# Performance work log

Measured on AMD Instinct MI355X. Metric: run time of the kernel, lower is better.

The kernel has to match this reference:

```python
import jax, jax.numpy as jnp
import numpy as np

N, E = 20000, 320000
C, IN_NF, HID_NF, OUT_NF, CH_NF, RAD_NF = 14, 128, 128, 128, 16, 128
CONSTANT = 1.0
LN_EPS = 1e-5
SCALE = 0.02


def _pool_matrix(c, dtype):
    # RollerPooling buffer: pool_matrix[i] averages a sliding window of size c-i
    ones = np.ones((c, c), dtype=np.float32)
    mats = [(np.triu(ones) - np.triu(ones, k=c - i)) / float(c - i) for i in range(c)]
    return jnp.asarray(np.stack(mats), dtype=dtype)


def setup_inputs() -> dict:
    key = jax.random.key(0)
    ks = jax.random.split(key, 32)
    h = jax.random.normal(ks[0], (N, IN_NF), jnp.float32)
    x = jax.random.normal(ks[1], (N, C, 3), jnp.float32)
    row = jax.random.randint(ks[2], (E,), 0, N)
    off = jax.random.randint(ks[3], (E,), 1, N)
    col = (row + off) % N  # guarantees row != col (avoids zero-distance edges)
    channel_attr = jax.random.normal(ks[4], (N, C, CH_NF), jnp.float32)
    w = jax.random.uniform(ks[5], (N, C), jnp.float32, 0.1, 1.0)
    keep = jax.random.uniform(ks[6], (N, C)) > 0.3
    keep = keep.at[:, 0].set(True)  # every node has >=1 active channel
    channel_weights = w * keep.astype(jnp.float32)

    def lin(k, o, i):
        k1, k2 = jax.random.split(k)
        return (jax.random.normal(k1, (o, i), jnp.float32) * SCALE,
                jax.random.normal(k2, (o,), jnp.float32) * SCALE)

    radial_W, radial_b = lin(ks[7], RAD_NF, CH_NF * CH_NF)
    e1_W, e1_b = lin(ks[8], HID_NF, 2 * IN_NF + RAD_NF)
    e2_W, e2_b = lin(ks[9], HID_NF, HID_NF)
    att_W, att_b = lin(ks[10], 1, HID_NF)
    c1_W, c1_b = lin(ks[11], HID_NF, HID_NF)
    c2_W, c2_b = lin(ks[12], C, HID_NF)
    n1_W, n1_b = lin(ks[13], HID_NF, IN_NF + HID_NF)
    n2_W, n2_b = lin(ks[14], OUT_NF, HID_NF)
    ln_g = jnp.ones((OUT_NF,), jnp.float32)
    ln_b = jnp.zeros((OUT_NF,), jnp.float32)
    return dict(h=h, x=x, row=row, col=col, channel_attr=channel_attr,
                channel_weights=channel_weights,
                radial_W=radial_W, radial_b=radial_b,
                e1_W=e1_W, e1_b=e1_b, e2_W=e2_W, e2_b=e2_b,
                att_W=att_W, att_b=att_b,
                c1_W=c1_W, c1_b=c1_b, c2_W=c2_W, c2_b=c2_b,
                n1_W=n1_W, n1_b=n1_b, n2_W=n2_W, n2_b=n2_b,
                ln_g=ln_g, ln_b=ln_b)


def _scatter_mean(v, idx, n):
    s = jnp.zeros((n,) + v.shape[1:], v.dtype).at[idx].add(v)
    cnt = jnp.zeros((n,), v.dtype).at[idx].add(1.0)
    cnt = jnp.maximum(cnt, 1.0)
    return s / cnt.reshape((n,) + (1,) * (v.ndim - 1))


def _forward(h, x, row, col, channel_attr, channel_weights,
             radial_W, radial_b, e1_W, e1_b, e2_W, e2_b, att_W, att_b,
             c1_W, c1_b, c2_W, c2_b, n1_W, n1_b, n2_W, n2_b, ln_g, ln_b):
    n, c, d = x.shape
    silu = jax.nn.silu
    coord_r = x[row]           # [E, C, 3]
    coord_c = x[col]
    # pairwise channel distances [E, C, C]
    dist = jnp.linalg.norm(coord_r[:, :, None, :] - coord_c[:, None, :, :], axis=-1)
    cw_r = channel_weights[row]
    cw_c = channel_weights[col]
    coord_msg = dist * (cw_r[:, :, None] * cw_c[:, None, :])
    # attr_r^T @ coord_msg @ attr_c -> [E, CH_NF, CH_NF]
    radial = jnp.einsum('eca,ecd,edb->eab', channel_attr[row], coord_msg, channel_attr[col])
    radial = radial.reshape(radial.shape[0], -1)
    rnorm = jnp.linalg.norm(radial, axis=-1, keepdims=True) + CONSTANT
    radial = (radial @ radial_W.T + radial_b) / rnorm  # [E, RAD_NF]
    # pooled column coord over active channels
    mask = (channel_weights != 0).astype(x.dtype)      # [N, C]
    csum = mask.sum(-1)                                # [N]
    pooled_col = (coord_c * mask[col][:, :, None]).sum(1) / csum[col][:, None]  # [E, 3]
    coord_diff = coord_r - pooled_col[:, None, :]      # [E, C, 3]
    # edge MLP (dropout = identity in eval)
    ef = jnp.concatenate([h[row], h[col], radial], axis=-1)
    ef = silu(ef @ e1_W.T + e1_b)
    ef = silu(ef @ e2_W.T + e2_b)
    ef = ef * jax.nn.sigmoid(ef @ att_W.T + att_b)     # att_mlp (hidden_nf == input_nf)
    # coord MLP + roller pooling
    ch = silu(ef @ c1_W.T + c1_b) @ c2_W.T + c2_b      # [E, C]
    tsize = csum[row].astype(jnp.int32) - 1            # [E] in [0, C-1]
    pool_mat = _pool_matrix(c, x.dtype)                # [C, C, C]
    pooled = jnp.einsum('eij,ej->ei', pool_mat[tsize], ch)  # [E, C]
    trans = coord_diff * pooled[:, :, None]            # [E, C, 3]
    x_out = x + _scatter_mean(trans, row, n)
    agg = _scatter_mean(ef, col, n)
    nh = jnp.concatenate([h, agg], axis=-1)
    nh = silu(nh @ n1_W.T + n1_b) @ n2_W.T + n2_b
    y = h + nh
    mu = y.mean(-1, keepdims=True)
    var = ((y - mu) ** 2).mean(-1, keepdims=True)
    h_out = (y - mu) / jnp.sqrt(var + LN_EPS) * ln_g + ln_b
    return h_out, x_out


def reference(h, x, row, col, channel_attr, channel_weights,
              radial_W, radial_b, e1_W, e1_b, e2_W, e2_b, att_W, att_b,
              c1_W, c1_b, c2_W, c2_b, n1_W, n1_b, n2_W, n2_b, ln_g, ln_b):
    return _forward(h, x, row, col, channel_attr, channel_weights,
                    radial_W, radial_b, e1_W, e1_b, e2_W, e2_b, att_W, att_b,
                    c1_W, c1_b, c2_W, c2_b, n1_W, n1_b, n2_W, n2_b, ln_g, ln_b)
```

## Files before the change

### kernel.cpp

```cpp
#include <hip/hip_runtime.h>
#include <math.h>

#define NN 20000
#define NE 320000

typedef const float* fp;
typedef short short8 __attribute__((ext_vector_type(8)));
typedef short short4v __attribute__((ext_vector_type(4)));
typedef float f32x4 __attribute__((ext_vector_type(4)));

__device__ __forceinline__ short F2B(float f) {
    unsigned u = __float_as_uint(f);
    return (short)((u + 0x7fffu + ((u >> 16) & 1u)) >> 16);
}
__device__ __forceinline__ short F2Bf(float f) {
    return (short)((__float_as_uint(f) + 0x8000u) >> 16);
}
__device__ __forceinline__ float B2F(short s) {
    return __uint_as_float(((unsigned)(unsigned short)s) << 16);
}
__device__ __forceinline__ float siluf(float v) { return v / (1.f + __expf(-v)); }
__device__ __forceinline__ f32x4 ld4(const float* p) {
    f32x4 v;
    __builtin_memcpy(&v, p, 16);
// ... 117 lines not shown
        wb[i] = F2B(v);
        return;
    }
    b -= 584;
    if (b < 128) {
        int o = b, k = tid;
        float acc = 0.f;
        for (int m = 0; m < 128; m++) acc += e1W[o * 384 + 256 + m] * rW[m * 256 + k];
        wb[32768 + o * 256 + k] = F2B(acc);
        if (k == 0) {
            float bsum = 0.f;
            for (int m = 0; m < 128; m++) bsum += e1W[o * 384 + 256 + m] * rB[m];
            bc[o] = bsum;
        }
        return;
    }
    b -= 128;
    if (b < 10000) {
        int i = b * 256 + tid;
        hb[i] = F2B(h[i]);
        return;
    }
    b -= 10000;
    if (b < 79) {
        int n = b * 256 + tid;
        if (n >= NN) return;
        float cnt = 0.f, px = 0.f, py = 0.f, pz = 0.f;
#pragma unroll
        for (int c = 0; c < 14; c++) {
            float w = cw[n * 14 + c];
            if (w != 0.f) {
                cnt += 1.f;
                px += x[(n * 14 + c) * 3 + 0];
                py += x[(n * 14 + c) * 3 + 1];
                pz += x[(n * 14 + c) * 3 + 2];
            }
        }
        if (cnt < 1.f) cnt = 1.f;
        csum[n] = cnt;
        pool[n * 3 + 0] = px / cnt;
        pool[n * 3 + 1] = py / cnt;
        pool[n * 3 + 2] = pz / cnt;
        return;
    }
    b -= 79;
    {
        int i = b * 256 + tid;
        int n = i >> 8, rem = i & 255, c = rem >> 4, a = rem & 15;
        float v = (c < 14) ? attr[(size_t)n * 224 + c * 16 + a] * cw[n * 14 + c] : 0.f;
        aT[(size_t)n * 256 + a * 16 + c] = F2B(v);
    }
}

__global__ void k_scan(int* __restrict__ cnt0, int* __restrict__ cnt1,
                       int* __restrict__ off0, int* __restrict__ off1) {
    __shared__ int part[256];
    const int tid = threadIdx.x;
    for (int a = 0; a < 2; a++) {
        int* cnt = a ? cnt1 : cnt0;
        int* off = a ? off1 : off0;
        int c0 = tid * 79, c1 = c0 + 79;
        if (c1 > 20000) c1 = 20000;
        int s = 0;
        for (int i = c0; i < c1; i++) s += cnt[i];
        part[tid] = s;
        __syncthreads();
        if (tid == 0) {
            int r = 0;
            for (int i = 0; i < 256; i++) { int t = part[i]; part[i] = r; r += t; }
        }
        __syncthreads();
        int run = part[tid];
        for (int i = c0; i < c1; i++) {
            int cv = cnt[i];
            off[i] = run;
            cnt[i] = run;
            run += cv;
        }
        if (tid == 255) off[20000] = run;
        __syncthreads();
    }
}

__global__ void k_fill(const int* __restrict__ row, const int* __restrict__ col,
                       int* __restrict__ head_r, int* __restrict__ head_c,
                       int* __restrict__ rpos,
                       int* __restrict__ row_s, int* __restrict__ col_s) {
    int e = blockIdx.x * 256 + threadIdx.x;
    if (e >= NE) return;
    int r = row[e], c = col[e];
    int pc = atomicAdd(&head_c[c], 1);
    row_s[pc] = r;
    col_s[pc] = c;
    int pr = atomicAdd(&head_r[r], 1);
    rpos[pc] = pr;
}

__device__ __forceinline__ void gemm_lds(const short* __restrict__ A, int sA,
                                         const short* __restrict__ W, int Ws, int K,
                                         int mt, int nt0, int nts, f32x4* acc) {
    const int lane = threadIdx.x & 63;
    const short* ap = A + (mt * 16 + (lane & 15)) * sA + ((lane >> 4) * 8);
    for (int k0 = 0; k0 < K; k0 += 32) {
        short8 a = *(const short8*)(ap + k0);
#pragma unroll
        for (int t = 0; t < nts; t++) {
            short8 b = *(const short8*)(W + ((nt0 + t) * 16 + (lane & 15)) * Ws + k0 + ((lane >> 4) * 8));
            acc[t] = __builtin_amdgcn_mfma_f32_16x16x32_bf16(a, b, acc[t], 0, 0, 0);
        }
    }
}
__device__ __forceinline__ void gemm_grow(const short* __restrict__ arow,
                                          const short* __restrict__ W, int Ws, int K,
                                          int nt0, int nts, f32x4* acc) {
    const int lane = threadIdx.x & 63;
    for (int k0 = 0; k0 < K; k0 += 32) {
        short8 a = *(const short8*)(arow + k0);
#pragma unroll
        for (int t = 0; t < nts; t++) {
            short8 b = *(const short8*)(W + ((nt0 + t) * 16 + (lane & 15)) * Ws + k0 + ((lane >> 4) * 8));
            acc[t] = __builtin_amdgcn_mfma_f32_16x16x32_bf16(a, b, acc[t], 0, 0, 0);
        }
    }
}

__global__ __launch_bounds__(256, 4) void k_hw(const short* __restrict__ hb,
                                               const short* __restrict__ wb,
                                               short* __restrict__ H12) {
    __shared__ __attribute__((aligned(16))) short A[32 * 136];
    const int tid = threadIdx.x, lane = tid & 63, w = tid >> 6;
    const int bb = lane & 15, quad = lane >> 4;
    const int mt = w & 1, nh = w >> 1, nb0 = blockIdx.x * 32;
    for (int p = tid; p < 512; p += 256) {
        int i = p >> 4, v = p & 15;
        *(short8*)(A + i * 136 + v * 8) = *(const short8*)(hb + (size_t)(nb0 + i) * 128 + v * 8);
    }
    __syncthreads();
    f32x4 acc[4];
#pragma unroll
    for (int t = 0; t < 4; t++) acc[t] = (f32x4){0.f, 0.f, 0.f, 0.f};
    gemm_lds(A, 136, wb, 256, 128, mt, nh * 4, 4, acc);
#pragma unroll
    for (int t = 0; t < 4; t++)
#pragma unroll
        for (int i = 0; i < 4; i++) {
            int m = mt * 16 + quad * 4 + i, n = (nh * 4 + t) * 16 + bb;
            H12[(size_t)(nb0 + m) * 256 + n] = F2Bf(acc[t][i]);
        }
#pragma unroll
    for (int t = 0; t < 4; t++) acc[t] = (f32x4){0.f, 0.f, 0.f, 0.f};
    gemm_lds(A, 136, wb + 128, 256, 128, mt, nh * 4, 4, acc);
#pragma unroll
    for (int t = 0; t < 4; t++)
#pragma unroll
        for (int i = 0; i < 4; i++) {
            int m = mt * 16 + quad * 4 + i, n = (nh * 4 + t) * 16 + bb;
            H12[(size_t)(nb0 + m) * 256 + 128 + n] = F2Bf(acc[t][i]);
        }
}

__global__ __launch_bounds__(256, 7) void k_edge(
    fp x, const int* __restrict__ row_s, const int* __restrict__ col_s,
    const int* __restrict__ rpos,
    const short* __restrict__ attrT, const short* __restrict__ H12,
    const short* __restrict__ wb, const float* __restrict__ bc,
    fp e1B, fp e2B, fp aW, fp aB, fp c1B, fp c2B,
    const float* __restrict__ csum, const float* __restrict__ poolc,
    short* __restrict__ e1p, short* __restrict__ pooledb,
    float* __restrict__ pcrec) {
    __shared__ __attribute__((aligned(16))) short U[8704];
    __shared__ float s_inv[32];
    __shared__ int s_r[32], s_c[32];
    __shared__ float s_ch[32][14];
    __shared__ float s_ps[32][15];
    __shared__ float s_red8[32][8], s_gate[32];

    const int tid = threadIdx.x, lane = tid & 63, w = tid >> 6;
    const int bb = lane & 15, quad = lane >> 4;
    const int mt = w & 1, nh = w >> 1;
    const int e0 = blockIdx.x * 32;
    const short* Wc = wb + 32768;
    short* Ar = U;
    short* V1 = U;
    short* V2 = U + 4352;

    if (tid < 32) { s_r[tid] = row_s[e0 + tid]; s_c[tid] = col_s[e0 + tid]; }
    __syncthreads();

    const int iic = bb < 14 ? bb : 13;
    const bool q3 = (quad == 3);
    const int cb = q3 ? 30 : quad * 12;
#pragma unroll 2
    for (int m = 0; m < 8; m++) {
        const int ei = w * 8 + m;
        const int r = s_r[ei], c = s_c[ei];
        short4v arv = *(const short4v*)(attrT + (size_t)r * 256 + bb * 16 + quad * 4);
        short4v acv = *(const short4v*)(attrT + (size_t)c * 256 + bb * 16 + quad * 4);
        const float* xrp = x + (size_t)r * 42 + iic * 3;
        float xr0 = xrp[0], xr1 = xrp[1], xr2 = xrp[2];
        const float* xcp = x + (size_t)c * 42 + cb;
        f32x4 L0 = ld4(xcp), L1 = ld4(xcp + 4), L2 = ld4(xcp + 8);
        float cxv[4], cyv[4], czv[4];
        cxv[0] = q3 ? L1[2] : L0[0]; cyv[0] = q3 ? L1[3] : L0[1]; czv[0] = q3 ? L2[0] : L0[2];
        cxv[1] = q3 ? L2[1] : L0[3]; cyv[1] = q3 ? L2[2] : L1[0]; czv[1] = q3 ? L2[3] : L1[1];
        cxv[2] = q3 ? L2[1] : L1[2]; cyv[2] = q3 ? L2[2] : L1[3]; czv[2] = q3 ? L2[3] : L2[0];
        cxv[3] = L2[1];              cyv[3] = L2[2];              czv[3] = L2[3];
        short4v msgv;
#pragma unroll
        for (int t = 0; t < 4; t++) {
            float dx = xr0 - cxv[t], dy = xr1 - cyv[t], dz = xr2 - czv[t];
            msgv[t] = F2Bf(sqrtf(dx * dx + dy * dy + dz * dz));
        }
        f32x4 t2 = mfma16(msgv, acv, (f32x4){0.f, 0.f, 0.f, 0.f});
        short4v t2v;
#pragma unroll
        for (int g = 0; g < 4; g++) t2v[g] = F2Bf(t2[g]);
        f32x4 rad = mfma16(arv, t2v, (f32x4){0.f, 0.f, 0.f, 0.f});
        float ss = rad[0] * rad[0] + rad[1] * rad[1] + rad[2] * rad[2] + rad[3] * rad[3];
#pragma unroll
        for (int off = 32; off > 0; off >>= 1) ss += __shfl_xor(ss, off, 64);
        float inv = 1.f / (sqrtf(ss) + 1.f);
        if (lane == 0) s_inv[ei] = inv;
#pragma unroll
        for (int g = 0; g < 4; g++)
            Ar[ei * 264 + (quad * 4 + g) * 16 + bb] = F2Bf(rad[g] * inv);
    }
    __syncthreads();

    f32x4 racc[2][2];
#pragma unroll
    for (int a = 0; a < 2; a++)
#pragma unroll
        for (int b = 0; b < 2; b++) racc[a][b] = (f32x4){0.f, 0.f, 0.f, 0.f};
    for (int k0 = 0; k0 < 256; k0 += 32) {
        short8 a0 = *(const short8*)(Ar + bb * 264 + k0 + quad * 8);
        short8 a1 = *(const short8*)(Ar + (16 + bb) * 264 + k0 + quad * 8);
        short8 b0 = *(const short8*)(Wc + (size_t)(w * 32 + bb) * 256 + k0 + quad * 8);
        short8 b1 = *(const short8*)(Wc + (size_t)(w * 32 + 16 + bb) * 256 + k0 + quad * 8);
        racc[0][0] = __builtin_amdgcn_mfma_f32_16x16x32_bf16(a0, b0, racc[0][0], 0, 0, 0);
        racc[0][1] = __builtin_amdgcn_mfma_f32_16x16x32_bf16(a0, b1, racc[0][1], 0, 0, 0);
        racc[1][0] = __builtin_amdgcn_mfma_f32_16x16x32_bf16(a1, b0, racc[1][0], 0, 0, 0);
        racc[1][1] = __builtin_amdgcn_mfma_f32_16x16x32_bf16(a1, b1, racc[1][1], 0, 0, 0);
    }
    __syncthreads();

#pragma unroll
    for (int a = 0; a < 2; a++)
#pragma unroll
        for (int b = 0; b < 2; b++)
#pragma unroll
            for (int i = 0; i < 4; i++) {
                int m = a * 16 + quad * 4 + i, n = w * 32 + b * 16 + bb;
                V1[m * 136 + n] = F2Bf(racc[a][b][i] + s_inv[m] * bc[n]);
            }
    __syncthreads();

    for (int p = tid; p < 512; p += 256) {
        int e = p >> 4, v = p & 15;
        short8 hr = *(const short8*)(H12 + (size_t)s_r[e] * 256 + v * 8);
        short8 hc = *(const short8*)(H12 + (size_t)s_c[e] * 256 + 128 + v * 8);
        short8 pp = *(const short8*)(V1 + e * 136 + v * 8);
        short8 o;
#pragma unroll
        for (int j = 0; j < 8; j++)
            o[j] = F2Bf(siluf(B2F(hr[j]) + B2F(hc[j]) + B2F(pp[j]) + e1B[v * 8 + j]));
        *(short8*)(V1 + e * 136 + v * 8) = o;
    }
    __syncthreads();

    f32x4 acc[4];
#pragma unroll
    for (int t = 0; t < 4; t++) acc[t] = (f32x4){0.f, 0.f, 0.f, 0.f};
    gemm_lds(V1, 136, wb + 65536, 128, 128, mt, nh * 4, 4, acc);
#pragma unroll
    for (int t = 0; t < 4; t++)
#pragma unroll
        for (int i = 0; i < 4; i++) {
            int m = mt * 16 + quad * 4 + i, n = (nh * 4 + t) * 16 + bb;
            V2[m * 136 + n] = F2Bf(siluf(acc[t][i] + e2B[n]));
        }
    __syncthreads();

    {
        int e = tid >> 3, j = tid & 7;
        float s = 0.f;
        for (int f = j * 16; f < j * 16 + 16; f++) s += B2F(V2[e * 136 + f]) * aW[f];
        s_red8[e][j] = s;
    }
    __syncthreads();
    if (tid < 32) {
        float s = 0.f;
#pragma unroll
        for (int j = 0; j < 8; j++) s += s_red8[tid][j];
        s_gate[tid] = 1.f / (1.f + __expf(-(s + aB[0])));
    }
#pragma unroll
    for (int t = 0; t < 4; t++) acc[t] = (f32x4){0.f, 0.f, 0.f, 0.f};
    gemm_lds(V2, 136, wb + 81920, 128, 128, mt, nh * 4, 4, acc);
    __syncthreads();

#pragma unroll
    for (int t = 0; t < 4; t++)
#pragma unroll
        for (int i = 0; i < 4; i++) {
            int m = mt * 16 + quad * 4 + i, n = (nh * 4 + t) * 16 + bb;
            V1[m * 136 + n] = F2Bf(siluf(s_gate[m] * acc[t][i] + c1B[n]));
        }
    for (int p = tid; p < 512; p += 256) {
        int e = p >> 4, v = p & 15;
        short8 a = *(const short8*)(V2 + e * 136 + v * 8);
        short8 o;
#pragma unroll
        for (int j = 0; j < 8; j++) o[j] = F2Bf(B2F(a[j]) * s_gate[e]);
        *(short8*)(e1p + (size_t)(e0 + e) * 128 + v * 8) = o;
    }
    __syncthreads();

    if (nh == 0) {
        f32x4 a4 = (f32x4){0.f, 0.f, 0.f, 0.f};
        gemm_lds(V1, 136, wb + 98304, 128, 128, mt, 0, 1, &a4);
#pragma unroll
        for (int i = 0; i < 4; i++) {
            int m = mt * 16 + quad * 4 + i;
            if (bb < 14) s_ch[m][bb] = a4[i] + c2B[bb];
        }
    }
    __syncthreads();

    if (tid < 32) {
        int t = (int)(csum[s_r[tid]] + 0.5f) - 1;
        if (t < 0) t = 0; if (t > 13) t = 13;
        int Wd = 14 - t;
        float run = 0.f;
        s_ps[tid][0] = 0.f;
        for (int j = 0; j < 14; j++) { run += s_ch[tid][j]; s_ps[tid][j + 1] = run; }
        float invW = 1.f / (float)Wd;
        int rp = rpos[e0 + tid];
        for (int i = 0; i < 14; i++) {
            int jend = i + Wd; if (jend > 14) jend = 14;
            pooledb[(size_t)rp * 14 + i] = F2Bf((s_ps[tid][jend] - s_ps[tid][i]) * invW);
        }
        int c = s_c[tid];
        float4 pc = make_float4(poolc[c * 3 + 0], poolc[c * 3 + 1], poolc[c * 3 + 2], 0.f);
        *(float4*)(pcrec + (size_t)rp * 4) = pc;
    }
}

__global__ __launch_bounds__(256, 3) void k_edge_fused(
    fp x, const int* __restrict__ row, const int* __restrict__ col,
    fp attr, fp cw, const short* __restrict__ hb, const short* __restrict__ wb,
    fp e1B, fp e2B, fp aW, fp aB, fp c1B, fp c2B,
    const float* __restrict__ bc, const float* __restrict__ csum,
    const float* __restrict__ poolc,
    float* __restrict__ xacc, float* __restrict__ agg,
    float* __restrict__ cntr, float* __restrict__ cntc) {
    __shared__ __attribute__((aligned(16))) short R1[13056];
    __shared__ float s_xr2[32 * 42];
    __shared__ float T[4][352];
    __shared__ int   s_r[32], s_c[32];
    __shared__ float s_inv[32];
    __shared__ float s_ch[32][14], s_pool[32][14];
    __shared__ float s_red8[32][8];
    __shared__ float s_gate[32];

    const int tid = threadIdx.x, lane = tid & 63, w = tid >> 6;
    const int bb = lane & 15, quad = lane >> 4;

    if (tid < 32) { s_r[tid] = row[blockIdx.x * 32 + tid]; s_c[tid] = col[blockIdx.x * 32 + tid]; }
    __syncthreads();

    float* slot = T[w];
    float* t2w = slot + 72;
    for (int i8 = 0; i8 < 8; i8++) {
        const int e = w * 8 + i8;
        const int r = s_r[e], cl = s_c[e];
        if (lane < 42) {
            s_xr2[e * 42 + lane] = x[(size_t)r * 42 + lane];
            slot[lane] = x[(size_t)cl * 42 + lane];
        }
        if (lane < 14)      slot[42 + lane] = cw[r * 14 + lane];
        else if (lane < 28) slot[56 + (lane - 14)] = cw[cl * 14 + (lane - 14)];
        __builtin_amdgcn_wave_barrier();

        const int iic = bb < 14 ? bb : 13;
        float xr0 = s_xr2[e * 42 + iic * 3], xr1 = s_xr2[e * 42 + iic * 3 + 1],
              xr2v = s_xr2[e * 42 + iic * 3 + 2];
        float cwri = slot[42 + iic];
        short8 msgv, acv;
#pragma unroll
        for (int t = 0; t < 8; t++) {
            int jj = quad * 8 + t, jc = jj < 14 ? jj : 13;
            float dx = xr0 - slot[jc * 3], dy = xr1 - slot[jc * 3 + 1], dz = xr2v - slot[jc * 3 + 2];
            float m = sqrtf(dx * dx + dy * dy + dz * dz) * cwri * slot[56 + jc];
            msgv[t] = (bb < 14 && jj < 14) ? F2B(m) : (short)0;
            acv[t] = F2B(attr[(size_t)cl * 224 + jc * 16 + bb]);
        }
        f32x4 t2 = (f32x4){0.f, 0.f, 0.f, 0.f};
        t2 = __builtin_amdgcn_mfma_f32_16x16x32_bf16(msgv, acv, t2, 0, 0, 0);
#pragma unroll
        for (int g = 0; g < 4; g++) t2w[(quad * 4 + g) * 17 + bb] = t2[g];
        __builtin_amdgcn_wave_barrier();

        short8 arv, t2v;
#pragma unroll
        for (int t = 0; t < 8; t++) {
            int kk = quad * 8 + t, kc = kk < 16 ? kk : 15;
            t2v[t] = F2B(t2w[kc * 17 + bb]);
            arv[t] = (kk < 14) ? F2B(attr[(size_t)r * 224 + kk * 16 + bb]) : (short)0;
        }
        f32x4 rad = (f32x4){0.f, 0.f, 0.f, 0.f};
        rad = __builtin_amdgcn_mfma_f32_16x16x32_bf16(arv, t2v, rad, 0, 0, 0);

// ... 39 lines not shown
    gemm_lds(V1, 136, wb + 65536, 128, 128, mt, nh * 4, 4, acc);
    __syncthreads();
#pragma unroll
    for (int t = 0; t < 4; t++)
#pragma unroll
        for (int i = 0; i < 4; i++) {
            int m = mt * 16 + quad * 4 + i, n = (nh * 4 + t) * 16 + bb;
            V2[m * 136 + n] = F2B(siluf(acc[t][i] + e2B[n]));
        }
    __syncthreads();

    {
        int e = tid >> 3, j = tid & 7;
        float s = 0.f;
        for (int f = j * 16; f < j * 16 + 16; f++) s += B2F(V2[e * 136 + f]) * aW[f];
        s_red8[e][j] = s;
    }
    __syncthreads();
    if (tid < 32) {
        float s = 0.f;
#pragma unroll
        for (int j = 0; j < 8; j++) s += s_red8[tid][j];
        s_gate[tid] = 1.f / (1.f + __expf(-(s + aB[0])));
    }
    __syncthreads();
    for (int p = tid; p < 32 * 128; p += 256) {
        int e = p >> 7, f = p & 127;
        V1[e * 136 + f] = F2B(B2F(V2[e * 136 + f]) * s_gate[e]);
    }
    __syncthreads();

#pragma unroll
    for (int t = 0; t < 4; t++) acc[t] = (f32x4){0.f, 0.f, 0.f, 0.f};
    gemm_lds(V1, 136, wb + 81920, 128, 128, mt, nh * 4, 4, acc);
    __syncthreads();
#pragma unroll
    for (int t = 0; t < 4; t++)
#pragma unroll
        for (int i = 0; i < 4; i++) {
            int m = mt * 16 + quad * 4 + i, n = (nh * 4 + t) * 16 + bb;
            C1O[m * 136 + n] = F2B(siluf(acc[t][i] + c1B[n]));
        }
    __syncthreads();

    if (nh == 0) {
        f32x4 a4 = (f32x4){0.f, 0.f, 0.f, 0.f};
        gemm_lds(C1O, 136, wb + 98304, 128, 128, mt, 0, 1, &a4);
#pragma unroll
        for (int i = 0; i < 4; i++) {
            int m = mt * 16 + quad * 4 + i;
            if (bb < 14) s_ch[m][bb] = a4[i] + c2B[bb];
        }
    }
    __syncthreads();

    if (tid < 32) {
        int t = (int)(csum[s_r[tid]] + 0.5f) - 1;
        if (t < 0) t = 0; if (t > 13) t = 13;
        int Wd = 14 - t;
        for (int i = 0; i < 14; i++) {
            int jend = i + Wd - 1; if (jend > 13) jend = 13;
            float a = 0.f;
            for (int j = i; j <= jend; j++) a += s_ch[tid][j];
            s_pool[tid][i] = a / (float)Wd;
        }
    }
    __syncthreads();

    for (int p = tid; p < 32 * 42; p += 256) {
        int e = p / 42, q = p - e * 42, i = q / 3, d = q - i * 3;
        float diff = s_xr2[e * 42 + q] - poolc[s_c[e] * 3 + d];
        atomicAdd(&xacc[(size_t)s_r[e] * 42 + q], diff * s_pool[e][i]);
    }
    for (int p = tid; p < 32 * 128; p += 256) {
        int e = p >> 7, f = p & 127;
        atomicAdd(&agg[(size_t)s_c[e] * 128 + f], B2F(V1[e * 136 + f]));
    }
    if (tid < 32) {
        atomicAdd(&cntr[s_r[tid]], 1.f);
        atomicAdd(&cntc[s_c[tid]], 1.f);
    }
}

__global__ __launch_bounds__(256, 4) void k_node_post_csr(
    fp h, fp x, const short* __restrict__ wb,
    fp n1B, fp n2B, fp lng, fp lnb,
    const short* __restrict__ efb, const short* __restrict__ pooledb,
    const int* __restrict__ off_c, const int* __restrict__ off_r,
    const float* __restrict__ pcrec,
    float* __restrict__ outh, float* __restrict__ outx) {
    __shared__ __attribute__((aligned(16))) short nA[32 * 264];
    __shared__ __attribute__((aligned(16))) short nMid[32 * 136];
    __shared__ float nred8[32][8];
    __shared__ float nmu[32], nrs[32];
    float* nY = (float*)nA;

    const int tid = threadIdx.x;
    const int wave = tid >> 6, mt = wave & 1, nh = wave >> 1;
    const int lane = tid & 63, bb = lane & 15, quad = lane >> 4;
    const int nb0 = blockIdx.x * 32;
    const short* n1Wb = wb + 100352;
    const short* n2Wb = wb + 133120;

    for (int p = tid; p < 32 * 128; p += 256) {
        int i = p >> 7, f = p & 127;
        nA[i * 264 + f] = F2Bf(h[(size_t)(nb0 + i) * 128 + f]);
    }
    {
        const int ni = tid >> 3, seg = tid & 7;
        const int n = nb0 + ni;
        const int beg = off_c[n], end = off_c[n + 1];
        float av[16];
#pragma unroll
        for (int j = 0; j < 16; j++) av[j] = 0.f;
        for (int k = beg; k < end; k++) {
            short8 u0 = *(const short8*)(efb + (size_t)k * 128 + seg * 16);
            short8 u1 = *(const short8*)(efb + (size_t)k * 128 + seg * 16 + 8);
#pragma unroll
            for (int j = 0; j < 8; j++) { av[j] += B2F(u0[j]); av[8 + j] += B2F(u1[j]); }
        }
        float inv = 1.f / fmaxf((float)(end - beg), 1.f);
#pragma unroll
        for (int j = 0; j < 16; j++)
            nA[ni * 264 + 128 + seg * 16 + j] = F2Bf(av[j] * inv);
    }
    __syncthreads();

    f32x4 acc[4];
#pragma unroll
    for (int t = 0; t < 4; t++) acc[t] = (f32x4){0.f, 0.f, 0.f, 0.f};
    gemm_lds(nA, 264, n1Wb, 256, 256, mt, nh * 4, 4, acc);
#pragma unroll
    for (int t = 0; t < 4; t++)
#pragma unroll
        for (int i = 0; i < 4; i++) {
            int m = mt * 16 + quad * 4 + i, n = (nh * 4 + t) * 16 + bb;
            nMid[m * 136 + n] = F2Bf(siluf(acc[t][i] + n1B[n]));
        }
    __syncthreads();

#pragma unroll
    for (int t = 0; t < 4; t++) acc[t] = (f32x4){0.f, 0.f, 0.f, 0.f};
    gemm_lds(nMid, 136, n2Wb, 128, 128, mt, nh * 4, 4, acc);
#pragma unroll
    for (int t = 0; t < 4; t++)
#pragma unroll
        for (int i = 0; i < 4; i++) {
            int m = mt * 16 + quad * 4 + i, n = (nh * 4 + t) * 16 + bb;
            nY[m * 128 + n] = acc[t][i] + n2B[n] + h[(size_t)(nb0 + m) * 128 + n];
        }
    __syncthreads();

    {
        int i = tid >> 3, j = tid & 7;
        float s = 0.f;
        for (int f = j * 16; f < j * 16 + 16; f++) s += nY[i * 128 + f];
        nred8[i][j] = s;
    }
    __syncthreads();
    if (tid < 32) {
        float s = 0.f;
#pragma unroll
        for (int j = 0; j < 8; j++) s += nred8[tid][j];
        nmu[tid] = s * (1.f / 128.f);
    }
    __syncthreads();
    {
        int i = tid >> 3, j = tid & 7;
        float mu = nmu[i], s = 0.f;
        for (int f = j * 16; f < j * 16 + 16; f++) { float d = nY[i * 128 + f] - mu; s += d * d; }
        nred8[i][j] = s;
    }
    __syncthreads();
    if (tid < 32) {
        float s = 0.f;
#pragma unroll
        for (int j = 0; j < 8; j++) s += nred8[tid][j];
        nrs[tid] = rsqrtf(s * (1.f / 128.f) + 1e-5f);
    }
    __syncthreads();
    for (int p = tid; p < 32 * 128; p += 256) {
        int i = p >> 7, f = p & 127;
        outh[(size_t)(nb0 + i) * 128 + f] = (nY[i * 128 + f] - nmu[i]) * nrs[i] * lng[f] + lnb[f];
    }
    for (int p = tid; p < 32 * 3; p += 256) {
        int i = p / 3, d = p - i * 3;
        int n = nb0 + i;
        int beg = off_r[n], end = off_r[n + 1];
        float Q[14], P[14];
#pragma unroll
        for (int ic = 0; ic < 14; ic++) { Q[ic] = 0.f; P[ic] = 0.f; }
        for (int k = beg; k < end; k++) {
            const int* pp = (const int*)(pooledb + (size_t)k * 14);
            float4 pc = *(const float4*)(pcrec + (size_t)k * 4);
            float pcd = (d == 0) ? pc.x : ((d == 1) ? pc.y : pc.z);
#pragma unroll
            for (int u2 = 0; u2 < 7; u2++) {
                int u = pp[u2];
                float pw0 = B2F((short)(u & 0xffff));
                float pw1 = B2F((short)(((unsigned)u) >> 16));
                P[2 * u2] += pw0;     Q[2 * u2] += pw0 * pcd;
                P[2 * u2 + 1] += pw1; Q[2 * u2 + 1] += pw1 * pcd;
            }
        }
        float invd = 1.f / fmaxf((float)(end - beg), 1.f);
#pragma unroll
        for (int ic = 0; ic < 14; ic++) {
            float x0 = x[(size_t)n * 42 + ic * 3 + d];
            outx[(size_t)n * 42 + ic * 3 + d] = x0 + (x0 * P[ic] - Q[ic]) * invd;
        }
    }
}

__global__ __launch_bounds__(256, 2) void k_node_post(
    fp h, fp x, const short* __restrict__ wb,
    fp n1B, fp n2B, fp lng, fp lnb,
    const float* __restrict__ agg, const float* __restrict__ cntc,
    const float* __restrict__ xacc, const float* __restrict__ cntr,
    float* __restrict__ outh, float* __restrict__ outx) {
    __shared__ __attribute__((aligned(16))) short nA[32 * 264];
    __shared__ __attribute__((aligned(16))) short nMid[32 * 136];
    __shared__ float nY[32][128];
    __shared__ float nred8[32][8];
    __shared__ float nmu[32], nrs[32];

    const int tid = threadIdx.x;
    const int wave = tid >> 6, mt = wave & 1, nh = wave >> 1;
    const int lane = tid & 63, bb = lane & 15, quad = lane >> 4;
    const int nb0 = blockIdx.x * 32;
    const short* n1Wb = wb + 100352;
    const short* n2Wb = wb + 133120;

    for (int p = tid; p < 32 * 128; p += 256) {
        int i = p >> 7, f = p & 127;
        int n = nb0 + i;
        nA[i * 264 + f] = F2Bf(h[(size_t)n * 128 + f]);
        float cc = cntc[n]; if (cc < 1.f) cc = 1.f;
        nA[i * 264 + 128 + f] = F2Bf(agg[(size_t)n * 128 + f] / cc);
    }
    __syncthreads();

    f32x4 acc[4];
#pragma unroll
    for (int t = 0; t < 4; t++) acc[t] = (f32x4){0.f, 0.f, 0.f, 0.f};
    gemm_lds(nA, 264, n1Wb, 256, 256, mt, nh * 4, 4, acc);
#pragma unroll
    for (int t = 0; t < 4; t++)
#pragma unroll
        for (int i = 0; i < 4; i++) {
            int m = mt * 16 + quad * 4 + i, n = (nh * 4 + t) * 16 + bb;
            nMid[m * 136 + n] = F2Bf(siluf(acc[t][i] + n1B[n]));
        }
    __syncthreads();

#pragma unroll
    for (int t = 0; t < 4; t++) acc[t] = (f32x4){0.f, 0.f, 0.f, 0.f};
    gemm_lds(nMid, 136, n2Wb, 128, 128, mt, nh * 4, 4, acc);
#pragma unroll
    for (int t = 0; t < 4; t++)
#pragma unroll
        for (int i = 0; i < 4; i++) {
            int m = mt * 16 + quad * 4 + i, n = (nh * 4 + t) * 16 + bb;
            nY[m][n] = acc[t][i] + n2B[n] + h[(size_t)(nb0 + m) * 128 + n];
        }
    __syncthreads();

    {
        int i = tid >> 3, j = tid & 7;
// ... 8 lines not shown
        for (int j = 0; j < 8; j++) s += nred8[tid][j];
        nmu[tid] = s * (1.f / 128.f);
    }
    __syncthreads();
    {
        int i = tid >> 3, j = tid & 7;
        float mu = nmu[i], s = 0.f;
        for (int f = j * 16; f < j * 16 + 16; f++) { float d = nY[i][f] - mu; s += d * d; }
        nred8[i][j] = s;
    }
    __syncthreads();
    if (tid < 32) {
        float s = 0.f;
#pragma unroll
        for (int j = 0; j < 8; j++) s += nred8[tid][j];
        nrs[tid] = rsqrtf(s * (1.f / 128.f) + 1e-5f);
    }
    __syncthreads();
    for (int p = tid; p < 32 * 128; p += 256) {
        int i = p >> 7, f = p & 127;
        outh[(size_t)(nb0 + i) * 128 + f] = (nY[i][f] - nmu[i]) * nrs[i] * lng[f] + lnb[f];
    }
    for (int p = tid; p < 32 * 42; p += 256) {
        int i = p / 42, q = p - i * 42;
        int n = nb0 + i;
        float cr = cntr[n]; if (cr < 1.f) cr = 1.f;
        outx[(size_t)n * 42 + q] = x[(size_t)n * 42 + q] + xacc[(size_t)n * 42 + q] / cr;
    }
}

extern "C" void kernel_launch(void* const* d_in, const int* in_sizes, int n_in,
                              void* d_out, int out_size, void* d_ws, size_t ws_size,
                              hipStream_t stream) {
    fp h   = (fp)d_in[0];
    fp x   = (fp)d_in[1];
    const int* row = (const int*)d_in[2];
    const int* col = (const int*)d_in[3];
    fp attr= (fp)d_in[4];
    fp cw  = (fp)d_in[5];
    fp rW  = (fp)d_in[6];  fp rB  = (fp)d_in[7];
    fp e1W = (fp)d_in[8];  fp e1B = (fp)d_in[9];
    fp e2W = (fp)d_in[10]; fp e2B = (fp)d_in[11];
    fp aW  = (fp)d_in[12]; fp aB  = (fp)d_in[13];
    fp c1W = (fp)d_in[14]; fp c1B = (fp)d_in[15];
    fp c2W = (fp)d_in[16]; fp c2B = (fp)d_in[17];
    fp n1W = (fp)d_in[18]; fp n1B = (fp)d_in[19];
    fp n2W = (fp)d_in[20]; fp n2B = (fp)d_in[21];
    fp lng = (fp)d_in[22]; fp lnb = (fp)d_in[23];

    float* ws    = (float*)d_ws;
    int*   wsi   = (int*)d_ws;
    float* xacc  = ws;
    float* agg   = ws + 840000;
    float* cntr  = ws + 3400000;
    float* cntc  = ws + 3420000;
    float* csum  = ws + 3440000;
    float* pool  = ws + 3460000;
    float* bc    = ws + 3520000;
    short* hb    = (short*)(ws + 3520128);
    short* wb    = (short*)(ws + 4800128);
    short* H12   = (short*)(ws + 4874880);
    short* e1p   = (short*)(ws + 7434880);
    short* attrT = (short*)(ws + 27914880);
    short* pooledb = (short*)(ws + 1040004);
    float* pcrec   = ws + 3520128;

    int* off_c  = wsi + 0;
    int* off_r  = wsi + 20002;
    int* head_c = wsi + 40004;
    int* head_r = wsi + 60004;
    int* rpos   = wsi + 80004;
    int* row_s  = wsi + 400004;
    int* col_s  = wsi + 720004;

    const size_t need = 30474880ull * 4ull;

    if (ws_size >= need) {
        hipMemsetAsync(head_c, 0, 40000 * sizeof(int), stream);
        k_prep_all<<<32041, 256, 0, stream>>>(e1W, e2W, c1W, c2W, n1W, n2W,
                                              rW, rB, h, x, attr, cw, row, col,
                                              wb, bc, hb, csum, pool, attrT,
                                              head_r, head_c);
        k_scan<<<1, 256, 0, stream>>>(head_c, head_r, off_c, off_r);
        k_fill<<<(NE + 255) / 256, 256, 0, stream>>>(row, col, head_r, head_c,
                                                     rpos, row_s, col_s);
        k_hw<<<NN / 32, 256, 0, stream>>>(hb, wb, H12);
        k_edge<<<NE / 32, 256, 0, stream>>>(x, row_s, col_s, rpos, attrT, H12, wb, bc,
                                            e1B, e2B, aW, aB, c1B, c2B,
                                            csum, pool, e1p, pooledb, pcrec);
        float* outh = (float*)d_out;
        float* outx = outh + NN * 128;
        k_node_post_csr<<<NN / 32, 256, 0, stream>>>(h, x, wb, n1B, n2B, lng, lnb,
                                                     e1p, pooledb,
                                                     off_c, off_r,
                                                     pcrec, outh, outx);
    } else {
        hipMemsetAsync(d_ws, 0, 3440000 * sizeof(float), stream);
        k_prep_w<<<(149504 + 255) / 256, 256, 0, stream>>>(e1W, e2W, c1W, c2W, n1W, n2W, wb);
        k_fold<<<128, 256, 0, stream>>>(e1W, rW, rB, wb, bc);
        k_prep_h<<<(NN * 128 + 255) / 256, 256, 0, stream>>>(h, hb);
        k_node_pre<<<(NN + 255) / 256, 256, 0, stream>>>(x, cw, csum, pool);
        k_edge_fused<<<NE / 32, 256, 0, stream>>>(x, row, col, attr, cw, hb, wb,
                                                  e1B, e2B, aW, aB, c1B, c2B,
                                                  bc, csum, pool, xacc, agg, cntr, cntc);
        float* outh = (float*)d_out;
        float* outx = outh + NN * 128;
        k_node_post<<<NN / 32, 256, 0, stream>>>(h, x, wb, n1B, n2B, lng, lnb,
                                                 agg, cntc, xacc, cntr, outh, outx);
    }
}
```

Before: 659.6 us.

## Merge fill and hw kernels; widen edge kernel to 64 edges per 512-thread block

The CSR fill and the node H12 GEMM are merged into one launch, split by block index, which removes a kernel launch and lets the two independent jobs overlap. The edge kernel now handles 64 edges per 512-thread block. Each wave loads one weight tile and reuses it across four row tiles in the radial GEMM. The gated e1p write-out now runs on the upper four waves while the lower four compute the coord projection, removing a barrier. The cost is double the LDS per block and possibly lower occupancy.

```diff
diff --git a/kernel.cpp b/kernel.cpp
--- a/kernel.cpp
+++ b/kernel.cpp
@@ -223,20 +223,6 @@
     }
 }
 
-__global__ void k_fill(const int* __restrict__ row, const int* __restrict__ col,
-                       int* __restrict__ head_r, int* __restrict__ head_c,
-                       int* __restrict__ rpos,
-                       int* __restrict__ row_s, int* __restrict__ col_s) {
-    int e = blockIdx.x * 256 + threadIdx.x;
-    if (e >= NE) return;
-    int r = row[e], c = col[e];
-    int pc = atomicAdd(&head_c[c], 1);
-    row_s[pc] = r;
-    col_s[pc] = c;
-    int pr = atomicAdd(&head_r[r], 1);
-    rpos[pc] = pr;
-}
-
 __device__ __forceinline__ void gemm_lds(const short* __restrict__ A, int sA,
                                          const short* __restrict__ W, int Ws, int K,
                                          int mt, int nt0, int nts, f32x4* acc) {
@@ -265,13 +251,29 @@
     }
 }
 
-__global__ __launch_bounds__(256, 4) void k_hw(const short* __restrict__ hb,
-                                               const short* __restrict__ wb,
-                                               short* __restrict__ H12) {
+__global__ __launch_bounds__(256, 4) void k_fill_hw(
+    const int* __restrict__ row, const int* __restrict__ col,
+    int* __restrict__ head_r, int* __restrict__ head_c,
+    int* __restrict__ rpos,
+    int* __restrict__ row_s, int* __restrict__ col_s,
+    const short* __restrict__ hb, const short* __restrict__ wb,
+    short* __restrict__ H12) {
     __shared__ __attribute__((aligned(16))) short A[32 * 136];
-    const int tid = threadIdx.x, lane = tid & 63, w = tid >> 6;
+    const int tid = threadIdx.x;
+    if (blockIdx.x < 1250) {
+        int e = blockIdx.x * 256 + tid;
+        if (e >= NE) return;
+        int r = row[e], c = col[e];
+        int pc = atomicAdd(&head_c[c], 1);
+        row_s[pc] = r;
+        col_s[pc] = c;
+        int pr = atomicAdd(&head_r[r], 1);
+        rpos[pc] = pr;
+        return;
+    }
+    const int lane = tid & 63, w = tid >> 6;
     const int bb = lane & 15, quad = lane >> 4;
-    const int mt = w & 1, nh = w >> 1, nb0 = blockIdx.x * 32;
+    const int mt = w & 1, nh = w >> 1, nb0 = (blockIdx.x - 1250) * 32;
     for (int p = tid; p < 512; p += 256) {
         int i = p >> 4, v = p & 15;
         *(short8*)(A + i * 136 + v * 8) = *(const short8*)(hb + (size_t)(nb0 + i) * 128 + v * 8);
@@ -300,7 +302,7 @@
         }
 }
 
-__global__ __launch_bounds__(256, 7) void k_edge(
+__global__ __launch_bounds__(512, 4) void k_edge(
     fp x, const int* __restrict__ row_s, const int* __restrict__ col_s,
     const int* __restrict__ rpos,
     const short* __restrict__ attrT, const short* __restrict__ H12,
@@ -309,23 +311,22 @@
     const float* __restrict__ csum, const float* __restrict__ poolc,
     short* __restrict__ e1p, short* __restrict__ pooledb,
     float* __restrict__ pcrec) {
-    __shared__ __attribute__((aligned(16))) short U[8704];
-    __shared__ float s_inv[32];
-    __shared__ int s_r[32], s_c[32];
-    __shared__ float s_ch[32][14];
-    __shared__ float s_ps[32][15];
-    __shared__ float s_red8[32][8], s_gate[32];
+    __shared__ __attribute__((aligned(16))) short U[17408];
+    __shared__ float s_inv[64];
+    __shared__ int s_r[64], s_c[64];
+    __shared__ float s_ch[64][14];
+    __shared__ float s_ps[64][15];
+    __shared__ float s_red8[64][8], s_gate[64];
 
     const int tid = threadIdx.x, lane = tid & 63, w = tid >> 6;
     const int bb = lane & 15, quad = lane >> 4;
-    const int mt = w & 1, nh = w >> 1;
-    const int e0 = blockIdx.x * 32;
+    const int e0 = blockIdx.x * 64;
     const short* Wc = wb + 32768;
     short* Ar = U;
     short* V1 = U;
-    short* V2 = U + 4352;
-
-    if (tid < 32) { s_r[tid] = row_s[e0 + tid]; s_c[tid] = col_s[e0 + tid]; }
+    short* V2 = U + 8704;
+
+    if (tid < 64) { s_r[tid] = row_s[e0 + tid]; s_c[tid] = col_s[e0 + tid]; }
     __syncthreads();
 
     const int iic = bb < 14 ? bb : 13;
@@ -368,35 +369,29 @@
     }
     __syncthreads();
 
-    f32x4 racc[2][2];
-#pragma unroll
-    for (int a = 0; a < 2; a++)
-#pragma unroll
-        for (int b = 0; b < 2; b++) racc[a][b] = (f32x4){0.f, 0.f, 0.f, 0.f};
+    f32x4 racc[4];
+#pragma unroll
+    for (int a = 0; a < 4; a++) racc[a] = (f32x4){0.f, 0.f, 0.f, 0.f};
     for (int k0 = 0; k0 < 256; k0 += 32) {
-        short8 a0 = *(const short8*)(Ar + bb * 264 + k0 + quad * 8);
-        short8 a1 = *(const short8*)(Ar + (16 + bb) * 264 + k0 + quad * 8);
-        short8 b0 = *(const short8*)(Wc + (size_t)(w * 32 + bb) * 256 + k0 + quad * 8);
-        short8 b1 = *(const short8*)(Wc + (size_t)(w * 32 + 16 + bb) * 256 + k0 + quad * 8);
-        racc[0][0] = __builtin_amdgcn_mfma_f32_16x16x32_bf16(a0, b0, racc[0][0], 0, 0, 0);
-        racc[0][1] = __builtin_amdgcn_mfma_f32_16x16x32_bf16(a0, b1, racc[0][1], 0, 0, 0);
-        racc[1][0] = __builtin_amdgcn_mfma_f32_16x16x32_bf16(a1, b0, racc[1][0], 0, 0, 0);
-        racc[1][1] = __builtin_amdgcn_mfma_f32_16x16x32_bf16(a1, b1, racc[1][1], 0, 0, 0);
-    }
-    __syncthreads();
-
-#pragma unroll
-    for (int a = 0; a < 2; a++)
-#pragma unroll
-        for (int b = 0; b < 2; b++)
-#pragma unroll
-            for (int i = 0; i < 4; i++) {
-                int m = a * 16 + quad * 4 + i, n = w * 32 + b * 16 + bb;
-                V1[m * 136 + n] = F2Bf(racc[a][b][i] + s_inv[m] * bc[n]);
-            }
-    __syncthreads();
-
-    for (int p = tid; p < 512; p += 256) {
+        short8 b = *(const short8*)(Wc + (size_t)(w * 16 + bb) * 256 + k0 + quad * 8);
+#pragma unroll
+        for (int a = 0; a < 4; a++) {
+            short8 av = *(const short8*)(Ar + (a * 16 + bb) * 264 + k0 + quad * 8);
+            racc[a] = __builtin_amdgcn_mfma_f32_16x16x32_bf16(av, b, racc[a], 0, 0, 0);
+        }
+    }
+    __syncthreads();
+
+#pragma unroll
+    for (int a = 0; a < 4; a++)
+#pragma unroll
+        for (int i = 0; i < 4; i++) {
+            int m = a * 16 + quad * 4 + i, n = w * 16 + bb;
+            V1[m * 136 + n] = F2Bf(racc[a][i] + s_inv[m] * bc[n]);
+        }
+    __syncthreads();
+
+    for (int p = tid; p < 1024; p += 512) {
         int e = p >> 4, v = p & 15;
         short8 hr = *(const short8*)(H12 + (size_t)s_r[e] * 256 + v * 8);
         short8 hc = *(const short8*)(H12 + (size_t)s_c[e] * 256 + 128 + v * 8);
@@ -409,6 +404,7 @@
     }
     __syncthreads();
 
+    const int mt = w & 3, nh = w >> 2;
     f32x4 acc[4];
 #pragma unroll
     for (int t = 0; t < 4; t++) acc[t] = (f32x4){0.f, 0.f, 0.f, 0.f};
@@ -429,7 +425,7 @@
         s_red8[e][j] = s;
     }
     __syncthreads();
-    if (tid < 32) {
+    if (tid < 64) {
         float s = 0.f;
 #pragma unroll
         for (int j = 0; j < 8; j++) s += s_red8[tid][j];
@@ -447,28 +443,29 @@
             int m = mt * 16 + quad * 4 + i, n = (nh * 4 + t) * 16 + bb;
             V1[m * 136 + n] = F2Bf(siluf(s_gate[m] * acc[t][i] + c1B[n]));
         }
-    for (int p = tid; p < 512; p += 256) {
-        int e = p >> 4, v = p & 15;
-        short8 a = *(const short8*)(V2 + e * 136 + v * 8);
-        short8 o;
-#pragma unroll
-        for (int j = 0; j < 8; j++) o[j] = F2Bf(B2F(a[j]) * s_gate[e]);
-        *(short8*)(e1p + (size_t)(e0 + e) * 128 + v * 8) = o;
-    }
-    __syncthreads();
-
-    if (nh == 0) {
+    __syncthreads();
+
+    if (w < 4) {
         f32x4 a4 = (f32x4){0.f, 0.f, 0.f, 0.f};
-        gemm_lds(V1, 136, wb + 98304, 128, 128, mt, 0, 1, &a4);
-#pragma unroll
-        for (int i = 0; i < 4; i++) {
-            int m = mt * 16 + quad * 4 + i;
+        gemm_lds(V1, 136, wb + 98304, 128, 128, w, 0, 1, &a4);
+#pragma unroll
+        for (int i = 0; i < 4; i++) {
+            int m = w * 16 + quad * 4 + i;
             if (bb < 14) s_ch[m][bb] = a4[i] + c2B[bb];
         }
-    }
-    __syncthreads();
-
-    if (tid < 32) {
+    } else {
+        for (int p = tid - 256; p < 1024; p += 256) {
+            int e = p >> 4, v = p & 15;
+            short8 a = *(const short8*)(V2 + e * 136 + v * 8);
+            short8 o;
+#pragma unroll
+            for (int j = 0; j < 8; j++) o[j] = F2Bf(B2F(a[j]) * s_gate[e]);
+            *(short8*)(e1p + (size_t)(e0 + e) * 128 + v * 8) = o;
+        }
+    }
+    __syncthreads();
+
+    if (tid < 64) {
         int t = (int)(csum[s_r[tid]] + 0.5f) - 1;
         if (t < 0) t = 0; if (t > 13) t = 13;
         int Wd = 14 - t;
@@ -950,10 +947,10 @@
                                               wb, bc, hb, csum, pool, attrT,
                                               head_r, head_c);
         k_scan<<<1, 256, 0, stream>>>(head_c, head_r, off_c, off_r);
-        k_fill<<<(NE + 255) / 256, 256, 0, stream>>>(row, col, head_r, head_c,
-                                                     rpos, row_s, col_s);
-        k_hw<<<NN / 32, 256, 0, stream>>>(hb, wb, H12);
-        k_edge<<<NE / 32, 256, 0, stream>>>(x, row_s, col_s, rpos, attrT, H12, wb, bc,
+        k_fill_hw<<<1250 + 625, 256, 0, stream>>>(row, col, head_r, head_c,
+                                                  rpos, row_s, col_s,
+                                                  hb, wb, H12);
+        k_edge<<<NE / 64, 512, 0, stream>>>(x, row_s, col_s, rpos, attrT, H12, wb, bc,
                                             e1B, e2B, aW, aB, c1B, c2B,
                                             csum, pool, e1p, pooledb, pcrec);
         float* outh = (float*)d_out;
```

Result: slower. 699.1 us (+6.0%).

## Merge fill and h-weight GEMM kernels; halve node-post tile to 16 nodes

Applied to the files above, without the earlier changes.

Combines the CSR fill kernel and the per-node h·W GEMM into one launch, with the first 1250 blocks doing the fill and the rest doing the GEMM. This removes a launch boundary and lets the two independent pieces of work overlap. The node post-processing kernel now handles 16 nodes per block instead of 32, which doubles the grid and raises the launch-bounds occupancy hint. The trade-off is that each wave has less MFMA work and weight reuse per block is lower.

```diff
diff --git a/kernel.cpp b/kernel.cpp
--- a/kernel.cpp
+++ b/kernel.cpp
@@ -223,20 +223,6 @@
     }
 }
 
-__global__ void k_fill(const int* __restrict__ row, const int* __restrict__ col,
-                       int* __restrict__ head_r, int* __restrict__ head_c,
-                       int* __restrict__ rpos,
-                       int* __restrict__ row_s, int* __restrict__ col_s) {
-    int e = blockIdx.x * 256 + threadIdx.x;
-    if (e >= NE) return;
-    int r = row[e], c = col[e];
-    int pc = atomicAdd(&head_c[c], 1);
-    row_s[pc] = r;
-    col_s[pc] = c;
-    int pr = atomicAdd(&head_r[r], 1);
-    rpos[pc] = pr;
-}
-
 __device__ __forceinline__ void gemm_lds(const short* __restrict__ A, int sA,
                                          const short* __restrict__ W, int Ws, int K,
                                          int mt, int nt0, int nts, f32x4* acc) {
@@ -265,13 +251,29 @@
     }
 }
 
-__global__ __launch_bounds__(256, 4) void k_hw(const short* __restrict__ hb,
-                                               const short* __restrict__ wb,
-                                               short* __restrict__ H12) {
+__global__ __launch_bounds__(256, 4) void k_fill_hw(
+    const int* __restrict__ row, const int* __restrict__ col,
+    int* __restrict__ head_r, int* __restrict__ head_c,
+    int* __restrict__ rpos,
+    int* __restrict__ row_s, int* __restrict__ col_s,
+    const short* __restrict__ hb, const short* __restrict__ wb,
+    short* __restrict__ H12) {
     __shared__ __attribute__((aligned(16))) short A[32 * 136];
-    const int tid = threadIdx.x, lane = tid & 63, w = tid >> 6;
+    const int tid = threadIdx.x;
+    if (blockIdx.x < 1250) {
+        int e = blockIdx.x * 256 + tid;
+        if (e >= NE) return;
+        int r = row[e], c = col[e];
+        int pc = atomicAdd(&head_c[c], 1);
+        row_s[pc] = r;
+        col_s[pc] = c;
+        int pr = atomicAdd(&head_r[r], 1);
+        rpos[pc] = pr;
+        return;
+    }
+    const int lane = tid & 63, w = tid >> 6;
     const int bb = lane & 15, quad = lane >> 4;
-    const int mt = w & 1, nh = w >> 1, nb0 = blockIdx.x * 32;
+    const int mt = w & 1, nh = w >> 1, nb0 = (blockIdx.x - 1250) * 32;
     for (int p = tid; p < 512; p += 256) {
         int i = p >> 4, v = p & 15;
         *(short8*)(A + i * 136 + v * 8) = *(const short8*)(hb + (size_t)(nb0 + i) * 128 + v * 8);
@@ -674,108 +676,107 @@
     }
 }
 
-__global__ __launch_bounds__(256, 4) void k_node_post_csr(
+__global__ __launch_bounds__(256, 6) void k_node_post_csr(
     fp h, fp x, const short* __restrict__ wb,
     fp n1B, fp n2B, fp lng, fp lnb,
     const short* __restrict__ efb, const short* __restrict__ pooledb,
     const int* __restrict__ off_c, const int* __restrict__ off_r,
     const float* __restrict__ pcrec,
     float* __restrict__ outh, float* __restrict__ outx) {
-    __shared__ __attribute__((aligned(16))) short nA[32 * 264];
-    __shared__ __attribute__((aligned(16))) short nMid[32 * 136];
-    __shared__ float nred8[32][8];
-    __shared__ float nmu[32], nrs[32];
+    __shared__ __attribute__((aligned(16))) short nA[16 * 264];
+    __shared__ __attribute__((aligned(16))) short nMid[16 * 136];
+    __shared__ float nred[16][16];
+    __shared__ float nmu[16], nrs[16];
     float* nY = (float*)nA;
 
     const int tid = threadIdx.x;
-    const int wave = tid >> 6, mt = wave & 1, nh = wave >> 1;
+    const int w = tid >> 6;
     const int lane = tid & 63, bb = lane & 15, quad = lane >> 4;
-    const int nb0 = blockIdx.x * 32;
+    const int nb0 = blockIdx.x * 16;
     const short* n1Wb = wb + 100352;
     const short* n2Wb = wb + 133120;
 
-    for (int p = tid; p < 32 * 128; p += 256) {
+    for (int p = tid; p < 16 * 128; p += 256) {
         int i = p >> 7, f = p & 127;
         nA[i * 264 + f] = F2Bf(h[(size_t)(nb0 + i) * 128 + f]);
     }
     {
-        const int ni = tid >> 3, seg = tid & 7;
+        const int ni = tid >> 4, seg = tid & 15;
         const int n = nb0 + ni;
         const int beg = off_c[n], end = off_c[n + 1];
-        float av[16];
-#pragma unroll
-        for (int j = 0; j < 16; j++) av[j] = 0.f;
+        float av[8];
+#pragma unroll
+        for (int j = 0; j < 8; j++) av[j] = 0.f;
         for (int k = beg; k < end; k++) {
-            short8 u0 = *(const short8*)(efb + (size_t)k * 128 + seg * 16);
-            short8 u1 = *(const short8*)(efb + (size_t)k * 128 + seg * 16 + 8);
-#pragma unroll
-            for (int j = 0; j < 8; j++) { av[j] += B2F(u0[j]); av[8 + j] += B2F(u1[j]); }
+            short8 u = *(const short8*)(efb + (size_t)k * 128 + seg * 8);
+#pragma unroll
+            for (int j = 0; j < 8; j++) av[j] += B2F(u[j]);
         }
         float inv = 1.f / fmaxf((float)(end - beg), 1.f);
 #pragma unroll
-        for (int j = 0; j < 16; j++)
-            nA[ni * 264 + 128 + seg * 16 + j] = F2Bf(av[j] * inv);
-    }
-    __syncthreads();
-
-    f32x4 acc[4];
-#pragma unroll
-    for (int t = 0; t < 4; t++) acc[t] = (f32x4){0.f, 0.f, 0.f, 0.f};
-    gemm_lds(nA, 264, n1Wb, 256, 256, mt, nh * 4, 4, acc);
-#pragma unroll
-    for (int t = 0; t < 4; t++)
-#pragma unroll
-        for (int i = 0; i < 4; i++) {
-            int m = mt * 16 + quad * 4 + i, n = (nh * 4 + t) * 16 + bb;
+        for (int j = 0; j < 8; j++)
+            nA[ni * 264 + 128 + seg * 8 + j] = F2Bf(av[j] * inv);
+    }
+    __syncthreads();
+
+    f32x4 acc[2];
+#pragma unroll
+    for (int t = 0; t < 2; t++) acc[t] = (f32x4){0.f, 0.f, 0.f, 0.f};
+    gemm_lds(nA, 264, n1Wb, 256, 256, 0, w * 2, 2, acc);
+#pragma unroll
+    for (int t = 0; t < 2; t++)
+#pragma unroll
+        for (int i = 0; i < 4; i++) {
+            int m = quad * 4 + i, n = (w * 2 + t) * 16 + bb;
             nMid[m * 136 + n] = F2Bf(siluf(acc[t][i] + n1B[n]));
         }
     __syncthreads();
 
 #pragma unroll
-    for (int t = 0; t < 4; t++) acc[t] = (f32x4){0.f, 0.f, 0.f, 0.f};
-    gemm_lds(nMid, 136, n2Wb, 128, 128, mt, nh * 4, 4, acc);
-#pragma unroll
-    for (int t = 0; t < 4; t++)
-#pragma unroll
-        for (int i = 0; i < 4; i++) {
-            int m = mt * 16 + quad * 4 + i, n = (nh * 4 + t) * 16 + bb;
+    for (int t = 0; t < 2; t++) acc[t] = (f32x4){0.f, 0.f, 0.f, 0.f};
+    gemm_lds(nMid, 136, n2Wb, 128, 128, 0, w * 2, 2, acc);
+#pragma unroll
+    for (int t = 0; t < 2; t++)
+#pragma unroll
+        for (int i = 0; i < 4; i++) {
+            int m = quad * 4 + i, n = (w * 2 + t) * 16 + bb;
             nY[m * 128 + n] = acc[t][i] + n2B[n] + h[(size_t)(nb0 + m) * 128 + n];
         }
     __syncthreads();
 
     {
-        int i = tid >> 3, j = tid & 7;
+        int i = tid >> 4, j = tid & 15;
         float s = 0.f;
-        for (int f = j * 16; f < j * 16 + 16; f++) s += nY[i * 128 + f];
-        nred8[i][j] = s;
-    }
-    __syncthreads();
-    if (tid < 32) {
+        for (int f = j * 8; f < j * 8 + 8; f++) s += nY[i * 128 + f];
+        nred[i][j] = s;
+    }
+    __syncthreads();
+    if (tid < 16) {
         float s = 0.f;
 #pragma unroll
-        for (int j = 0; j < 8; j++) s += nred8[tid][j];
+        for (int j = 0; j < 16; j++) s += nred[tid][j];
         nmu[tid] = s * (1.f / 128.f);
     }
     __syncthreads();
     {
-        int i = tid >> 3, j = tid & 7;
+        int i = tid >> 4, j = tid & 15;
         float mu = nmu[i], s = 0.f;
-        for (int f = j * 16; f < j * 16 + 16; f++) { float d = nY[i * 128 + f] - mu; s += d * d; }
-        nred8[i][j] = s;
-    }
-    __syncthreads();
-    if (tid < 32) {
+        for (int f = j * 8; f < j * 8 + 8; f++) { float d = nY[i * 128 + f] - mu; s += d * d; }
+        nred[i][j] = s;
+    }
+    __syncthreads();
+    if (tid < 16) {
         float s = 0.f;
 #pragma unroll
-        for (int j = 0; j < 8; j++) s += nred8[tid][j];
+        for (int j = 0; j < 16; j++) s += nred[tid][j];
         nrs[tid] = rsqrtf(s * (1.f / 128.f) + 1e-5f);
     }
     __syncthreads();
-    for (int p = tid; p < 32 * 128; p += 256) {
+    for (int p = tid; p < 16 * 128; p += 256) {
         int i = p >> 7, f = p & 127;
         outh[(size_t)(nb0 + i) * 128 + f] = (nY[i * 128 + f] - nmu[i]) * nrs[i] * lng[f] + lnb[f];
     }
-    for (int p = tid; p < 32 * 3; p += 256) {
+    for (int p = tid; p < 16 * 3; p += 256) {
         int i = p / 3, d = p - i * 3;
         int n = nb0 + i;
         int beg = off_r[n], end = off_r[n + 1];
@@ -950,15 +951,15 @@
                                               wb, bc, hb, csum, pool, attrT,
                                               head_r, head_c);
         k_scan<<<1, 256, 0, stream>>>(head_c, head_r, off_c, off_r);
-        k_fill<<<(NE + 255) / 256, 256, 0, stream>>>(row, col, head_r, head_c,
-                                                     rpos, row_s, col_s);
-        k_hw<<<NN / 32, 256, 0, stream>>>(hb, wb, H12);
+        k_fill_hw<<<1250 + 625, 256, 0, stream>>>(row, col, head_r, head_c,
+                                                  rpos, row_s, col_s,
+                                                  hb, wb, H12);
         k_edge<<<NE / 32, 256, 0, stream>>>(x, row_s, col_s, rpos, attrT, H12, wb, bc,
                                             e1B, e2B, aW, aB, c1B, c2B,
                                             csum, pool, e1p, pooledb, pcrec);
         float* outh = (float*)d_out;
         float* outx = outh + NN * 128;
-        k_node_post_csr<<<NN / 32, 256, 0, stream>>>(h, x, wb, n1B, n2B, lng, lnb,
+        k_node_post_csr<<<NN / 16, 256, 0, stream>>>(h, x, wb, n1B, n2B, lng, lnb,
                                                      e1p, pooledb,
                                                      off_c, off_r,
                                                      pcrec, outh, outx);
```

Measured after the change: 658.9 us, median of 2. No clear change (-0.1%).
